# Kernel tuning notes

Measured on AMD Instinct MI355X. Metric: run time of the kernel, lower is better.

Reference implementation:

```python
import jax, jax.numpy as jnp
import numpy as np

NIN = 1024
NOUT = 1024
NHEADS = 16
DHEAD = NOUT // NHEADS


def setup_inputs() -> dict:
    key = jax.random.key(0)
    k1, k2, k3, k4 = jax.random.split(key, 4)
    y = jax.random.normal(k1, (2, 2048, NIN), dtype=jnp.float32)
    Wqkv = jax.random.normal(k2, (NIN, 3 * NOUT), dtype=jnp.float32) * (1.0 / np.sqrt(NIN))
    Wff = jax.random.normal(k3, (NOUT, NOUT), dtype=jnp.float32) * (1.0 / np.sqrt(NOUT))
    bff = jax.random.normal(k4, (NOUT,), dtype=jnp.float32) * 0.01
    return {"y": y, "Wqkv": Wqkv, "Wff": Wff, "bff": bff}


def reference(y, Wqkv, Wff, bff):
    b, n, _ = y.shape
    qkv = y @ Wqkv  # [b, n, 3*nout]
    qkv = qkv.reshape(b, n, 3, NHEADS, DHEAD).transpose(2, 0, 3, 1, 4)
    q, k, v = qkv[0], qkv[1], qkv[2]  # each [b, h, n, d]
    att = jnp.einsum('bhqd,bhkd->bhqk', q, k)
    causal = jnp.triu(jnp.ones((n, n), dtype=bool), k=1)
    att = jnp.where(causal, -jnp.inf, att)
    att = jax.nn.softmax(att / jnp.sqrt(jnp.float32(DHEAD)), axis=-1)
    ctx = jnp.einsum('bhqk,bhkd->bhqd', att, v)
    ctx = ctx.transpose(0, 2, 1, 3).reshape(b, n, NOUT)
    return ctx @ Wff + bff
```

## Files before the change

### kernel.cpp

```cpp
#include <hip/hip_runtime.h>
#include <stdint.h>

#define NHEADS 16
#define DHEAD 64
#define SEQ 2048
#define BATCH 2
#define NINF 1024
#define NOUTF 1024
#define N3 3072
#define MTOT 4096

typedef unsigned short US;
typedef __attribute__((ext_vector_type(8))) short short8;
typedef __attribute__((ext_vector_type(4))) short short4v;
typedef __attribute__((ext_vector_type(4))) float f32x4;

__device__ inline US f2bf(float f) {
  union { float f; unsigned u; } v; v.f = f;
  unsigned r = v.u + 0x7fffu + ((v.u >> 16) & 1u);
  return (US)(r >> 16);
}

__device__ inline f32x4 mfma16(short8 a, short8 b, f32x4 c) {
  return __builtin_amdgcn_mfma_f32_16x16x32_bf16(a, b, c, 0, 0, 0);
}

__device__ inline f32x4 mfma16k16(short4v a, short4v b, f32x4 c) {
  return __builtin_amdgcn_mfma_f32_16x16x16bf16_1k(a, b, c, 0, 0, 0);
}

__device__ inline void async16(const US* g, US* l) {
  __builtin_amdgcn_global_load_lds(
      (const __attribute__((address_space(1))) unsigned int*)g,
      (__attribute__((address_space(3))) unsigned int*)l, 16, 0, 0);
}

__global__ void k_convert(const float* __restrict__ src, US* __restrict__ dst, int n4) {
  int i = blockIdx.x * blockDim.x + threadIdx.x;
  if (i >= n4) return;
  float4 v = ((const float4*)src)[i];
  ushort4 o;
  o.x = f2bf(v.x); o.y = f2bf(v.y); o.z = f2bf(v.z); o.w = f2bf(v.w);
  ((ushort4*)dst)[i] = o;
}

__global__ void k_wtrans(const float* __restrict__ Wqkv, const float* __restrict__ Wff,
                         US* __restrict__ dq, US* __restrict__ df) {
  __shared__ float tile[32][33];
  int bxi = blockIdx.x;
  const float* src; US* dst; int C;
  if (bxi < 96) { src = Wqkv; dst = dq; C = N3; }
  else          { src = Wff;  dst = df; C = NOUTF; bxi -= 96; }
  int bx = bxi * 32, by = blockIdx.y * 32;
  int tx = threadIdx.x, ty = threadIdx.y;
  for (int i = 0; i < 32; i += 8)
    tile[ty + i][tx] = src[(size_t)(by + ty + i) * C + bx + tx];
  __syncthreads();
  for (int i = 0; i < 32; i += 8)
    dst[(size_t)(bx + ty + i) * 1024 + by + tx] = f2bf(tile[tx][ty + i]);
}

__global__ void k_vtrans(const US* __restrict__ src, US* __restrict__ dst) {
  __shared__ US tile[32][33];
  int bh = blockIdx.z;
  int bx = blockIdx.x * 32;
  int by = blockIdx.y * 32;
  int tx = threadIdx.x, ty = threadIdx.y;
  const US* s0 = src + (size_t)bh * SEQ * DHEAD;
  US* d0 = dst + (size_t)bh * DHEAD * SEQ;
  for (int i = 0; i < 32; i += 8)
    tile[ty + i][tx] = s0[(size_t)(by + ty + i) * DHEAD + bx + tx];
  __syncthreads();
  for (int i = 0; i < 32; i += 8)
    d0[(size_t)(bx + ty + i) * SEQ + by + tx] = tile[tx][ty + i];
}

__global__ __launch_bounds__(256) void k_gemm_qkv(
    const US* __restrict__ A,
    const US* __restrict__ Bt,
    US* __restrict__ qbuf, US* __restrict__ kbuf, US* __restrict__ vbuf) {
  __shared__ US As[128 * 32];
  __shared__ US Bs[128 * 32];
  int tid = threadIdx.x;
  int wave = tid >> 6, lane = tid & 63, lm = lane & 15, lk = lane >> 4;
  int wm = wave >> 1, wn = wave & 1;
  int mbase = blockIdx.y * 128, nbase = blockIdx.x * 128;

  f32x4 acc[4][4];
#pragma unroll
  for (int i = 0; i < 4; ++i)
#pragma unroll
    for (int j = 0; j < 4; ++j) acc[i][j] = (f32x4){0.f, 0.f, 0.f, 0.f};

  const US* ga = A + (size_t)(mbase + (tid >> 2)) * NINF + (tid & 3) * 8;
  const US* gb = Bt + (size_t)(nbase + (tid >> 2)) * NINF + (tid & 3) * 8;
  US* la = As + tid * 8;
  US* lb = Bs + tid * 8;

  for (int kt = 0; kt < NINF / 32; ++kt) {
    int ko = kt * 32;
    async16(ga + ko, la);
    async16(ga + ko + (size_t)64 * NINF, la + 64 * 32);
    async16(gb + ko, lb);
    async16(gb + ko + (size_t)64 * NINF, lb + 64 * 32);
    __syncthreads();
    short8 a[4], b[4];
#pragma unroll
    for (int i = 0; i < 4; ++i)
      a[i] = *(const short8*)(As + (wm * 64 + i * 16 + lm) * 32 + lk * 8);
#pragma unroll
    for (int j = 0; j < 4; ++j)
      b[j] = *(const short8*)(Bs + (wn * 64 + j * 16 + lm) * 32 + lk * 8);
#pragma unroll
    for (int i = 0; i < 4; ++i)
#pragma unroll
      for (int j = 0; j < 4; ++j) acc[i][j] = mfma16(a[i], b[j], acc[i][j]);
    __syncthreads();
  }

  int which = nbase >> 10;
  US* dsts = (which == 0) ? qbuf : (which == 1) ? kbuf : vbuf;
  float sc = (which == 0) ? 0.18033688011112042f : 1.f;
#pragma unroll
  for (int j = 0; j < 4; ++j) {
    int col = nbase + wn * 64 + j * 16 + lm;
    int hh = (col & 1023) >> 6;
    int d = col & 63;
#pragma unroll
    for (int i = 0; i < 4; ++i) {
#pragma unroll
      for (int r = 0; r < 4; ++r) {
        int row = mbase + wm * 64 + i * 16 + lk * 4 + r;
        int bb = row >> 11;
        int s = row & (SEQ - 1);
        int bh = bb * NHEADS + hh;
        dsts[((size_t)bh * SEQ + s) * DHEAD + d] = f2bf(acc[i][j][r] * sc);
      }
    }
  }
}

__global__ __launch_bounds__(256) void k_attn(
    const US* __restrict__ qbuf, const US* __restrict__ kbuf,
    const US* __restrict__ vtbuf, US* __restrict__ ctx) {
  __shared__ US Ks[64 * 64];
  __shared__ US Vs[64 * 64];
  int tid = threadIdx.x;
  int w = tid >> 6, lane = tid & 63;
  int lm = lane & 15, lk = lane >> 4;
  int bl = blockIdx.x;
  int xcd = bl & 7, g = bl >> 3;
  int bh = (g & 3) * 8 + xcd;
  int s = 31 - (g >> 2);
  int qb = s * 64 + w * 16;
  int nt = s + 1;

  const US* kbase = kbuf + (size_t)bh * SEQ * DHEAD;
  const US* vtb = vtbuf + (size_t)bh * DHEAD * SEQ;
  const US* qr = qbuf + ((size_t)bh * SEQ + qb + lm) * DHEAD + lk * 8;
  short8 qf0 = *(const short8*)(qr);
  short8 qf1 = *(const short8*)(qr + 32);

  int swz = ((lane & 7) ^ (lane >> 3)) * 8;
  const US* gsrc[4];
  US* ldst[4];
  int step[4];
#pragma unroll
  for (int j = 0; j < 4; ++j) {
    int u = w + 4 * j;
    if (u < 8) {
      gsrc[j] = kbase + (size_t)(u * 8 + (lane >> 3)) * DHEAD + swz;
      ldst[j] = Ks + u * 512 + lane * 8;
      step[j] = 64 * DHEAD;
    } else {
      int i = u - 8;
      gsrc[j] = vtb + (size_t)(i * 8 + (lane >> 3)) * SEQ + swz;
      ldst[j] = Vs + i * 512 + lane * 8;
      step[j] = 64;
    }
  }

  int xorv = lm & 7;
  int ck0 = ((lk) ^ xorv) * 16;
  int ck1 = ((4 + lk) ^ xorv) * 16;
  int cv[4];
#pragma unroll
  for (int kg = 0; kg < 4; ++kg)
    cv[kg] = (((kg * 2 + (lk >> 1)) ^ xorv) * 16) + (lk & 1) * 8;

  f32x4 o[4];
#pragma unroll
  for (int dg = 0; dg < 4; ++dg) o[dg] = (f32x4){0.f, 0.f, 0.f, 0.f};
  f32x4 lacc = (f32x4){0.f, 0.f, 0.f, 0.f};
  const short4v kones = {(short)0x3F80, (short)0x3F80, (short)0x3F80, (short)0x3F80};

  const char* Kc = (const char*)Ks;
  const char* Vc = (const char*)Vs;

  auto body = [&](int kg, bool dm) {
    const char* kr = Kc + (kg * 16 + lm) * 128;
    short8 ka0 = *(const short8*)(kr + ck0);
    short8 ka1 = *(const short8*)(kr + ck1);
    f32x4 st = (f32x4){0.f, 0.f, 0.f, 0.f};
    st = mfma16(ka0, qf0, st);
    st = mfma16(ka1, qf1, st);
    uint32_t ue[4];
#pragma unroll
    for (int r = 0; r < 4; ++r) {
      float v = st[r];
      if (dm && (lk * 4 + r > lm)) v = -INFINITY;
      union { float f; uint32_t u; } cv2;
      cv2.f = exp2f(v);
      ue[r] = cv2.u + 0x8000u;
    }
    union { short4v s4; uint32_t u[2]; } pk;
    pk.u[0] = __builtin_amdgcn_perm(ue[1], ue[0], 0x07060302u);
    pk.u[1] = __builtin_amdgcn_perm(ue[3], ue[2], 0x07060302u);
    lacc = mfma16k16(kones, pk.s4, lacc);
    const char* vr = Vc + lm * 128 + cv[kg];
#pragma unroll
    for (int dg = 0; dg < 4; ++dg) {
      short4v va = *(const short4v*)(vr + dg * 2048);
      o[dg] = mfma16k16(va, pk.s4, o[dg]);
    }
  };

  for (int t = 0; t < nt - 1; ++t) {
    __syncthreads();
#pragma unroll
    for (int j = 0; j < 4; ++j) async16(gsrc[j], ldst[j]);
#pragma unroll
    for (int j = 0; j < 4; ++j) gsrc[j] += step[j];
    __syncthreads();
#pragma unroll
    for (int kg = 0; kg < 4; ++kg) body(kg, false);
  }
  __syncthreads();
#pragma unroll
  for (int j = 0; j < 4; ++j) async16(gsrc[j], ldst[j]);
  __syncthreads();
  for (int kg = 0; kg < w; ++kg) body(kg, false);
  body(w, true);

  float inv = 1.f / lacc[0];

  US* crow = ctx + ((size_t)(bh >> 4) * SEQ + qb + lm) * NOUTF + (bh & 15) * DHEAD;
#pragma unroll
  for (int dg = 0; dg < 4; ++dg) {
    union { short4v s4; uint32_t u[2]; } pk;
    pk.u[0] = (uint32_t)f2bf(o[dg][0] * inv) | ((uint32_t)f2bf(o[dg][1] * inv) << 16);
    pk.u[1] = (uint32_t)f2bf(o[dg][2] * inv) | ((uint32_t)f2bf(o[dg][3] * inv) << 16);
    *(short4v*)(crow + dg * 16 + lk * 4) = pk.s4;
  }
}

__global__ __launch_bounds__(256) void k_gemm_out(
    const US* __restrict__ A, const US* __restrict__ Bt,
    const float* __restrict__ bias, float* __restrict__ out) {
  __shared__ US As[128 * 32];
  __shared__ US Bs[64 * 32];
  int tid = threadIdx.x;
  int wave = tid >> 6, lane = tid & 63, lm = lane & 15, lk = lane >> 4;
  int mbase = blockIdx.y * 128, nbase = blockIdx.x * 64;

  f32x4 acc[2][4];
#pragma unroll
  for (int i = 0; i < 2; ++i)
#pragma unroll
    for (int j = 0; j < 4; ++j) acc[i][j] = (f32x4){0.f, 0.f, 0.f, 0.f};

  const US* ga = A + (size_t)(mbase + (tid >> 2)) * NOUTF + (tid & 3) * 8;
  const US* gb = Bt + (size_t)(nbase + (tid >> 2)) * NOUTF + (tid & 3) * 8;
  US* la = As + tid * 8;
  US* lb = Bs + tid * 8;

  for (int kt = 0; kt < NOUTF / 32; ++kt) {
    int ko = kt * 32;
    async16(ga + ko, la);
    async16(ga + ko + (size_t)64 * NOUTF, la + 64 * 32);
    async16(gb + ko, lb);
    __syncthreads();
    short8 a[2], b[4];
#pragma unroll
    for (int i = 0; i < 2; ++i)
      a[i] = *(const short8*)(As + (wave * 32 + i * 16 + lm) * 32 + lk * 8);
#pragma unroll
    for (int j = 0; j < 4; ++j)
      b[j] = *(const short8*)(Bs + (j * 16 + lm) * 32 + lk * 8);
#pragma unroll
    for (int i = 0; i < 2; ++i)
#pragma unroll
      for (int j = 0; j < 4; ++j) acc[i][j] = mfma16(a[i], b[j], acc[i][j]);
    __syncthreads();
  }

#pragma unroll
  for (int j = 0; j < 4; ++j) {
    int col = nbase + j * 16 + lm;
    float bv = bias[col];
#pragma unroll
    for (int i = 0; i < 2; ++i)
#pragma unroll
      for (int r = 0; r < 4; ++r) {
        int row = mbase + wave * 32 + i * 16 + lk * 4 + r;
        out[(size_t)row * NOUTF + col] = acc[i][j][r] + bv;
      }
  }
}

extern "C" void kernel_launch(void* const* d_in, const int* in_sizes, int n_in,
                              void* d_out, int out_size, void* d_ws, size_t ws_size,
                              hipStream_t stream) {
  const float* y    = (const float*)d_in[0];
  const float* Wqkv = (const float*)d_in[1];
  const float* Wff  = (const float*)d_in[2];
  const float* bff  = (const float*)d_in[3];
  float* out = (float*)d_out;

  char* ws = (char*)d_ws;
  US* ybf   = (US*)(ws);
  US* ctx   = (US*)(ws);
  US* wqkvt = (US*)(ws + (8u << 20));
  US* wfft  = (US*)(ws + (14u << 20));
  US* qbuf  = (US*)(ws + (16u << 20));
  US* kbuf  = (US*)(ws + (24u << 20));
  US* vbuf  = (US*)(ws + (32u << 20));
  US* vtbuf = (US*)(ws + (40u << 20));

  k_convert<<<MTOT * NINF / 4 / 256, 256, 0, stream>>>(y, ybf, MTOT * NINF / 4);
  k_wtrans<<<dim3(128, 32), dim3(32, 8), 0, stream>>>(Wqkv, Wff, wqkvt, wfft);
  k_gemm_qkv<<<dim3(N3 / 128, MTOT / 128), 256, 0, stream>>>(ybf, wqkvt, qbuf, kbuf, vbuf);
  k_vtrans<<<dim3(DHEAD / 32, SEQ / 32, BATCH * NHEADS), dim3(32, 8), 0, stream>>>(vbuf, vtbuf);
  k_attn<<<dim3(1024), 256, 0, stream>>>(qbuf, kbuf, vtbuf, ctx);
  k_gemm_out<<<dim3(NOUTF / 64, MTOT / 128), 256, 0, stream>>>(ctx, wfft, bff, out);
}
```

Before: 191.7 us.

## Double-buffer K/V tiles and pair causal query tiles per attention block

```diff
diff --git a/kernel.cpp b/kernel.cpp
--- a/kernel.cpp
+++ b/kernel.cpp
@@ -143,114 +143,127 @@
 __global__ __launch_bounds__(256) void k_attn(
     const US* __restrict__ qbuf, const US* __restrict__ kbuf,
     const US* __restrict__ vtbuf, US* __restrict__ ctx) {
-  __shared__ US Ks[64 * 64];
-  __shared__ US Vs[64 * 64];
+  __shared__ US Ks[2][64 * 64];
+  __shared__ US Vs[2][64 * 64];
   int tid = threadIdx.x;
   int w = tid >> 6, lane = tid & 63;
   int lm = lane & 15, lk = lane >> 4;
   int bl = blockIdx.x;
   int xcd = bl & 7, g = bl >> 3;
   int bh = (g & 3) * 8 + xcd;
-  int s = 31 - (g >> 2);
-  int qb = s * 64 + w * 16;
-  int nt = s + 1;
+  int p = g >> 2;
 
   const US* kbase = kbuf + (size_t)bh * SEQ * DHEAD;
   const US* vtb = vtbuf + (size_t)bh * DHEAD * SEQ;
-  const US* qr = qbuf + ((size_t)bh * SEQ + qb + lm) * DHEAD + lk * 8;
-  short8 qf0 = *(const short8*)(qr);
-  short8 qf1 = *(const short8*)(qr + 32);
+  const US* q_base = qbuf + (size_t)bh * SEQ * DHEAD;
+  US* cbase = ctx + (size_t)(bh >> 4) * SEQ * NOUTF + (bh & 15) * DHEAD;
 
   int swz = ((lane & 7) ^ (lane >> 3)) * 8;
-  const US* gsrc[4];
-  US* ldst[4];
-  int step[4];
-#pragma unroll
-  for (int j = 0; j < 4; ++j) {
-    int u = w + 4 * j;
-    if (u < 8) {
-      gsrc[j] = kbase + (size_t)(u * 8 + (lane >> 3)) * DHEAD + swz;
-      ldst[j] = Ks + u * 512 + lane * 8;
-      step[j] = 64 * DHEAD;
-    } else {
-      int i = u - 8;
-      gsrc[j] = vtb + (size_t)(i * 8 + (lane >> 3)) * SEQ + swz;
-      ldst[j] = Vs + i * 512 + lane * 8;
-      step[j] = 64;
+  int u = w;
+  const US* gK0[2]; const US* gV0[2];
+  US* dK[2][2]; US* dV[2][2];
+#pragma unroll
+  for (int j = 0; j < 2; ++j) {
+    int uk = w + 4 * j;
+    int uv = w + 4 * j;
+    gK0[j] = kbase + (size_t)(uk * 8 + (lane >> 3)) * DHEAD + swz;
+    gV0[j] = vtb + (size_t)(uv * 8 + (lane >> 3)) * SEQ + swz;
+#pragma unroll
+    for (int b = 0; b < 2; ++b) {
+      dK[b][j] = Ks[b] + uk * 512 + lane * 8;
+      dV[b][j] = Vs[b] + uv * 512 + lane * 8;
     }
   }
+  (void)u;
 
   int xorv = lm & 7;
   int ck0 = ((lk) ^ xorv) * 16;
   int ck1 = ((4 + lk) ^ xorv) * 16;
-  int cv[4];
-#pragma unroll
-  for (int kg = 0; kg < 4; ++kg)
-    cv[kg] = (((kg * 2 + (lk >> 1)) ^ xorv) * 16) + (lk & 1) * 8;
-
-  f32x4 o[4];
-#pragma unroll
-  for (int dg = 0; dg < 4; ++dg) o[dg] = (f32x4){0.f, 0.f, 0.f, 0.f};
-  f32x4 lacc = (f32x4){0.f, 0.f, 0.f, 0.f};
   const short4v kones = {(short)0x3F80, (short)0x3F80, (short)0x3F80, (short)0x3F80};
 
-  const char* Kc = (const char*)Ks;
-  const char* Vc = (const char*)Vs;
-
-  auto body = [&](int kg, bool dm) {
-    const char* kr = Kc + (kg * 16 + lm) * 128;
-    short8 ka0 = *(const short8*)(kr + ck0);
-    short8 ka1 = *(const short8*)(kr + ck1);
-    f32x4 st = (f32x4){0.f, 0.f, 0.f, 0.f};
-    st = mfma16(ka0, qf0, st);
-    st = mfma16(ka1, qf1, st);
-    uint32_t ue[4];
-#pragma unroll
-    for (int r = 0; r < 4; ++r) {
-      float v = st[r];
-      if (dm && (lk * 4 + r > lm)) v = -INFINITY;
-      union { float f; uint32_t u; } cv2;
-      cv2.f = exp2f(v);
-      ue[r] = cv2.u + 0x8000u;
+  for (int half = 0; half < 2; ++half) {
+    int s = half ? p : (31 - p);
+    int qb = s * 64 + w * 16;
+    int nt = s + 1;
+
+    const US* qr = q_base + (size_t)(qb + lm) * DHEAD + lk * 8;
+    short8 qf0 = *(const short8*)(qr);
+    short8 qf1 = *(const short8*)(qr + 32);
+
+    f32x4 o[4];
+#pragma unroll
+    for (int dg = 0; dg < 4; ++dg) o[dg] = (f32x4){0.f, 0.f, 0.f, 0.f};
+    f32x4 lacc = (f32x4){0.f, 0.f, 0.f, 0.f};
+
+    const US* gK[2]; const US* gV[2];
+#pragma unroll
+    for (int j = 0; j < 2; ++j) { gK[j] = gK0[j]; gV[j] = gV0[j]; }
+
+#pragma unroll
+    for (int j = 0; j < 2; ++j) { async16(gK[j], dK[0][j]); async16(gV[j], dV[0][j]); }
+#pragma unroll
+    for (int j = 0; j < 2; ++j) { gK[j] += 64 * DHEAD; gV[j] += 64; }
+    __syncthreads();
+
+    for (int t = 0; t < nt; ++t) {
+      int cur = t & 1, nxt = cur ^ 1;
+      if (t + 1 < nt) {
+#pragma unroll
+        for (int j = 0; j < 2; ++j) { async16(gK[j], dK[nxt][j]); async16(gV[j], dV[nxt][j]); }
+#pragma unroll
+        for (int j = 0; j < 2; ++j) { gK[j] += 64 * DHEAD; gV[j] += 64; }
+      }
+
+      const char* Kc = (const char*)Ks[cur];
+      const char* Vc = (const char*)Vs[cur];
+      auto body = [&](int kg, bool dm) {
+        const char* kr = Kc + (kg * 16 + lm) * 128;
+        short8 ka0 = *(const short8*)(kr + ck0);
+        short8 ka1 = *(const short8*)(kr + ck1);
+        f32x4 st = (f32x4){0.f, 0.f, 0.f, 0.f};
+        st = mfma16(ka0, qf0, st);
+        st = mfma16(ka1, qf1, st);
+        uint32_t ue[4];
+#pragma unroll
+        for (int r = 0; r < 4; ++r) {
+          float v = st[r];
+          if (dm && (lk * 4 + r > lm)) v = -INFINITY;
+          union { float f; uint32_t u; } cv2;
+          cv2.f = exp2f(v);
+          ue[r] = cv2.u + 0x8000u;
+        }
+        union { short4v s4; uint32_t u[2]; } pk;
+        pk.u[0] = __builtin_amdgcn_perm(ue[1], ue[0], 0x07060302u);
+        pk.u[1] = __builtin_amdgcn_perm(ue[3], ue[2], 0x07060302u);
+        lacc = mfma16k16(kones, pk.s4, lacc);
+        int cvo = (((kg * 2 + (lk >> 1)) ^ xorv) * 16) + (lk & 1) * 8;
+        const char* vr = Vc + lm * 128 + cvo;
+#pragma unroll
+        for (int dg = 0; dg < 4; ++dg) {
+          short4v va = *(const short4v*)(vr + dg * 2048);
+          o[dg] = mfma16k16(va, pk.s4, o[dg]);
+        }
+      };
+
+      if (t == nt - 1) {
+        for (int kg = 0; kg < w; ++kg) body(kg, false);
+        body(w, true);
+      } else {
+#pragma unroll
+        for (int kg = 0; kg < 4; ++kg) body(kg, false);
+      }
+      __syncthreads();
     }
-    union { short4v s4; uint32_t u[2]; } pk;
-    pk.u[0] = __builtin_amdgcn_perm(ue[1], ue[0], 0x07060302u);
-    pk.u[1] = __builtin_amdgcn_perm(ue[3], ue[2], 0x07060302u);
-    lacc = mfma16k16(kones, pk.s4, lacc);
-    const char* vr = Vc + lm * 128 + cv[kg];
+
+    float inv = 1.f / lacc[0];
+    US* crow = cbase + (size_t)(qb + lm) * NOUTF;
 #pragma unroll
     for (int dg = 0; dg < 4; ++dg) {
-      short4v va = *(const short4v*)(vr + dg * 2048);
-      o[dg] = mfma16k16(va, pk.s4, o[dg]);
+      union { short4v s4; uint32_t u[2]; } pk;
+      pk.u[0] = (uint32_t)f2bf(o[dg][0] * inv) | ((uint32_t)f2bf(o[dg][1] * inv) << 16);
+      pk.u[1] = (uint32_t)f2bf(o[dg][2] * inv) | ((uint32_t)f2bf(o[dg][3] * inv) << 16);
+      *(short4v*)(crow + dg * 16 + lk * 4) = pk.s4;
     }
-  };
-
-  for (int t = 0; t < nt - 1; ++t) {
-    __syncthreads();
-#pragma unroll
-    for (int j = 0; j < 4; ++j) async16(gsrc[j], ldst[j]);
-#pragma unroll
-    for (int j = 0; j < 4; ++j) gsrc[j] += step[j];
-    __syncthreads();
-#pragma unroll
-    for (int kg = 0; kg < 4; ++kg) body(kg, false);
-  }
-  __syncthreads();
-#pragma unroll
-  for (int j = 0; j < 4; ++j) async16(gsrc[j], ldst[j]);
-  __syncthreads();
-  for (int kg = 0; kg < w; ++kg) body(kg, false);
-  body(w, true);
-
-  float inv = 1.f / lacc[0];
-
-  US* crow = ctx + ((size_t)(bh >> 4) * SEQ + qb + lm) * NOUTF + (bh & 15) * DHEAD;
-#pragma unroll
-  for (int dg = 0; dg < 4; ++dg) {
-    union { short4v s4; uint32_t u[2]; } pk;
-    pk.u[0] = (uint32_t)f2bf(o[dg][0] * inv) | ((uint32_t)f2bf(o[dg][1] * inv) << 16);
-    pk.u[1] = (uint32_t)f2bf(o[dg][2] * inv) | ((uint32_t)f2bf(o[dg][3] * inv) << 16);
-    *(short4v*)(crow + dg * 16 + lk * 4) = pk.s4;
   }
 }
 
@@ -331,6 +344,6 @@
   k_wtrans<<<dim3(128, 32), dim3(32, 8), 0, stream>>>(Wqkv, Wff, wqkvt, wfft);
   k_gemm_qkv<<<dim3(N3 / 128, MTOT / 128), 256, 0, stream>>>(ybf, wqkvt, qbuf, kbuf, vbuf);
   k_vtrans<<<dim3(DHEAD / 32, SEQ / 32, BATCH * NHEADS), dim3(32, 8), 0, stream>>>(vbuf, vtbuf);
-  k_attn<<<dim3(1024), 256, 0, stream>>>(qbuf, kbuf, vtbuf, ctx);
+  k_attn<<<dim3(512), 256, 0, stream>>>(qbuf, kbuf, vtbuf, ctx);
   k_gemm_out<<<dim3(NOUTF / 64, MTOT / 128), 256, 0, stream>>>(ctx, wfft, bff, out);
 }
```

New measurement: 194.8 us. No clear change (+1.6%).

## Have each attention wave process two 16-row query groups to reuse K/V fragments

Applied to the files above, without the earlier changes.

```diff
diff --git a/kernel.cpp b/kernel.cpp
--- a/kernel.cpp
+++ b/kernel.cpp
@@ -14,6 +14,12 @@
 typedef __attribute__((ext_vector_type(8))) short short8;
 typedef __attribute__((ext_vector_type(4))) short short4v;
 typedef __attribute__((ext_vector_type(4))) float f32x4;
+
+#if __has_builtin(__builtin_amdgcn_exp2f)
+#define EXP2(x) __builtin_amdgcn_exp2f(x)
+#else
+#define EXP2(x) exp2f(x)
+#endif
 
 __device__ inline US f2bf(float f) {
   union { float f; unsigned u; } v; v.f = f;
@@ -140,7 +146,7 @@
   }
 }
 
-__global__ __launch_bounds__(256) void k_attn(
+__global__ __launch_bounds__(128, 2) void k_attn(
     const US* __restrict__ qbuf, const US* __restrict__ kbuf,
     const US* __restrict__ vtbuf, US* __restrict__ ctx) {
   __shared__ US Ks[64 * 64];
@@ -149,108 +155,121 @@
   int w = tid >> 6, lane = tid & 63;
   int lm = lane & 15, lk = lane >> 4;
   int bl = blockIdx.x;
-  int xcd = bl & 7, g = bl >> 3;
-  int bh = (g & 3) * 8 + xcd;
-  int s = 31 - (g >> 2);
-  int qb = s * 64 + w * 16;
+  int xcd = bl & 7, g2 = bl >> 3;
+  int bh = (g2 & 3) * 8 + xcd;
+  int s = 31 - (g2 >> 2);
+  int qb = s * 64 + w * 32;
   int nt = s + 1;
 
   const US* kbase = kbuf + (size_t)bh * SEQ * DHEAD;
   const US* vtb = vtbuf + (size_t)bh * DHEAD * SEQ;
-  const US* qr = qbuf + ((size_t)bh * SEQ + qb + lm) * DHEAD + lk * 8;
-  short8 qf0 = *(const short8*)(qr);
-  short8 qf1 = *(const short8*)(qr + 32);
+  const US* q_base = qbuf + (size_t)bh * SEQ * DHEAD;
+
+  short8 qf[2][2];
+#pragma unroll
+  for (int g = 0; g < 2; ++g) {
+    const US* qr = q_base + (size_t)(qb + g * 16 + lm) * DHEAD + lk * 8;
+    qf[g][0] = *(const short8*)(qr);
+    qf[g][1] = *(const short8*)(qr + 32);
+  }
 
   int swz = ((lane & 7) ^ (lane >> 3)) * 8;
-  const US* gsrc[4];
-  US* ldst[4];
-  int step[4];
+  const US* gK[4]; const US* gV[4];
+  US* dKl[4]; US* dVl[4];
 #pragma unroll
   for (int j = 0; j < 4; ++j) {
-    int u = w + 4 * j;
-    if (u < 8) {
-      gsrc[j] = kbase + (size_t)(u * 8 + (lane >> 3)) * DHEAD + swz;
-      ldst[j] = Ks + u * 512 + lane * 8;
-      step[j] = 64 * DHEAD;
-    } else {
-      int i = u - 8;
-      gsrc[j] = vtb + (size_t)(i * 8 + (lane >> 3)) * SEQ + swz;
-      ldst[j] = Vs + i * 512 + lane * 8;
-      step[j] = 64;
-    }
+    int u = w * 4 + j;
+    gK[j] = kbase + (size_t)(u * 8 + (lane >> 3)) * DHEAD + swz;
+    dKl[j] = Ks + u * 512 + lane * 8;
+    gV[j] = vtb + (size_t)(u * 8 + (lane >> 3)) * SEQ + swz;
+    dVl[j] = Vs + u * 512 + lane * 8;
   }
 
   int xorv = lm & 7;
   int ck0 = ((lk) ^ xorv) * 16;
   int ck1 = ((4 + lk) ^ xorv) * 16;
-  int cv[4];
-#pragma unroll
-  for (int kg = 0; kg < 4; ++kg)
-    cv[kg] = (((kg * 2 + (lk >> 1)) ^ xorv) * 16) + (lk & 1) * 8;
-
-  f32x4 o[4];
-#pragma unroll
-  for (int dg = 0; dg < 4; ++dg) o[dg] = (f32x4){0.f, 0.f, 0.f, 0.f};
-  f32x4 lacc = (f32x4){0.f, 0.f, 0.f, 0.f};
   const short4v kones = {(short)0x3F80, (short)0x3F80, (short)0x3F80, (short)0x3F80};
+
+  f32x4 o[2][4];
+#pragma unroll
+  for (int g = 0; g < 2; ++g)
+#pragma unroll
+    for (int dg = 0; dg < 4; ++dg) o[g][dg] = (f32x4){0.f, 0.f, 0.f, 0.f};
+  f32x4 lacc[2];
+  lacc[0] = (f32x4){0.f, 0.f, 0.f, 0.f};
+  lacc[1] = (f32x4){0.f, 0.f, 0.f, 0.f};
 
   const char* Kc = (const char*)Ks;
   const char* Vc = (const char*)Vs;
 
-  auto body = [&](int kg, bool dm) {
+  auto body = [&](int kg, bool act0, bool dm0, bool dm1) {
     const char* kr = Kc + (kg * 16 + lm) * 128;
     short8 ka0 = *(const short8*)(kr + ck0);
     short8 ka1 = *(const short8*)(kr + ck1);
-    f32x4 st = (f32x4){0.f, 0.f, 0.f, 0.f};
-    st = mfma16(ka0, qf0, st);
-    st = mfma16(ka1, qf1, st);
-    uint32_t ue[4];
-#pragma unroll
-    for (int r = 0; r < 4; ++r) {
-      float v = st[r];
-      if (dm && (lk * 4 + r > lm)) v = -INFINITY;
-      union { float f; uint32_t u; } cv2;
-      cv2.f = exp2f(v);
-      ue[r] = cv2.u + 0x8000u;
-    }
-    union { short4v s4; uint32_t u[2]; } pk;
-    pk.u[0] = __builtin_amdgcn_perm(ue[1], ue[0], 0x07060302u);
-    pk.u[1] = __builtin_amdgcn_perm(ue[3], ue[2], 0x07060302u);
-    lacc = mfma16k16(kones, pk.s4, lacc);
-    const char* vr = Vc + lm * 128 + cv[kg];
+    short4v pk[2];
+    bool act[2] = {act0, true};
+    bool dm[2] = {dm0, dm1};
+#pragma unroll
+    for (int g = 0; g < 2; ++g) {
+      if (!act[g]) continue;
+      f32x4 st = (f32x4){0.f, 0.f, 0.f, 0.f};
+      st = mfma16(ka0, qf[g][0], st);
+      st = mfma16(ka1, qf[g][1], st);
+      uint32_t ue[4];
+#pragma unroll
+      for (int r = 0; r < 4; ++r) {
+        float v = st[r];
+        if (dm[g] && (lk * 4 + r > lm)) v = -INFINITY;
+        union { float f; uint32_t u; } cv2;
+        cv2.f = EXP2(v);
+        ue[r] = cv2.u + 0x8000u;
+      }
+      union { short4v s4; uint32_t u[2]; } pz;
+      pz.u[0] = __builtin_amdgcn_perm(ue[1], ue[0], 0x07060302u);
+      pz.u[1] = __builtin_amdgcn_perm(ue[3], ue[2], 0x07060302u);
+      pk[g] = pz.s4;
+      lacc[g] = mfma16k16(kones, pk[g], lacc[g]);
+    }
+    int cvo = (((kg * 2 + (lk >> 1)) ^ xorv) * 16) + (lk & 1) * 8;
+    const char* vr = Vc + lm * 128 + cvo;
 #pragma unroll
     for (int dg = 0; dg < 4; ++dg) {
       short4v va = *(const short4v*)(vr + dg * 2048);
-      o[dg] = mfma16k16(va, pk.s4, o[dg]);
+      if (act0) o[0][dg] = mfma16k16(va, pk[0], o[0][dg]);
+      o[1][dg] = mfma16k16(va, pk[1], o[1][dg]);
     }
   };
 
-  for (int t = 0; t < nt - 1; ++t) {
-    __syncthreads();
-#pragma unroll
-    for (int j = 0; j < 4; ++j) async16(gsrc[j], ldst[j]);
-#pragma unroll
-    for (int j = 0; j < 4; ++j) gsrc[j] += step[j];
-    __syncthreads();
-#pragma unroll
-    for (int kg = 0; kg < 4; ++kg) body(kg, false);
-  }
-  __syncthreads();
-#pragma unroll
-  for (int j = 0; j < 4; ++j) async16(gsrc[j], ldst[j]);
-  __syncthreads();
-  for (int kg = 0; kg < w; ++kg) body(kg, false);
-  body(w, true);
-
-  float inv = 1.f / lacc[0];
-
-  US* crow = ctx + ((size_t)(bh >> 4) * SEQ + qb + lm) * NOUTF + (bh & 15) * DHEAD;
-#pragma unroll
-  for (int dg = 0; dg < 4; ++dg) {
-    union { short4v s4; uint32_t u[2]; } pk;
-    pk.u[0] = (uint32_t)f2bf(o[dg][0] * inv) | ((uint32_t)f2bf(o[dg][1] * inv) << 16);
-    pk.u[1] = (uint32_t)f2bf(o[dg][2] * inv) | ((uint32_t)f2bf(o[dg][3] * inv) << 16);
-    *(short4v*)(crow + dg * 16 + lk * 4) = pk.s4;
+  for (int t = 0; t < nt; ++t) {
+    __syncthreads();
+#pragma unroll
+    for (int j = 0; j < 4; ++j) { async16(gK[j], dKl[j]); async16(gV[j], dVl[j]); }
+#pragma unroll
+    for (int j = 0; j < 4; ++j) { gK[j] += 64 * DHEAD; gV[j] += 64; }
+    __syncthreads();
+
+    if (t < nt - 1) {
+#pragma unroll
+      for (int kg = 0; kg < 4; ++kg) body(kg, true, false, false);
+    } else {
+      int kmax = 2 * w + 1;
+      for (int kg = 0; kg <= kmax; ++kg)
+        body(kg, kg <= 2 * w, kg == 2 * w, kg == kmax);
+    }
+  }
+
+  US* cb = ctx + (size_t)(bh >> 4) * SEQ * NOUTF + (bh & 15) * DHEAD;
+#pragma unroll
+  for (int g = 0; g < 2; ++g) {
+    float inv = 1.f / lacc[g][0];
+    US* crow = cb + (size_t)(qb + g * 16 + lm) * NOUTF;
+#pragma unroll
+    for (int dg = 0; dg < 4; ++dg) {
+      union { short4v s4; uint32_t u[2]; } pz;
+      pz.u[0] = (uint32_t)f2bf(o[g][dg][0] * inv) | ((uint32_t)f2bf(o[g][dg][1] * inv) << 16);
+      pz.u[1] = (uint32_t)f2bf(o[g][dg][2] * inv) | ((uint32_t)f2bf(o[g][dg][3] * inv) << 16);
+      *(short4v*)(crow + dg * 16 + lk * 4) = pz.s4;
+    }
   }
 }
 
@@ -331,6 +350,6 @@
   k_wtrans<<<dim3(128, 32), dim3(32, 8), 0, stream>>>(Wqkv, Wff, wqkvt, wfft);
   k_gemm_qkv<<<dim3(N3 / 128, MTOT / 128), 256, 0, stream>>>(ybf, wqkvt, qbuf, kbuf, vbuf);
   k_vtrans<<<dim3(DHEAD / 32, SEQ / 32, BATCH * NHEADS), dim3(32, 8), 0, stream>>>(vbuf, vtbuf);
-  k_attn<<<dim3(1024), 256, 0, stream>>>(qbuf, kbuf, vtbuf, ctx);
+  k_attn<<<dim3(1024), 128, 0, stream>>>(qbuf, kbuf, vtbuf, ctx);
   k_gemm_out<<<dim3(NOUTF / 64, MTOT / 128), 256, 0, stream>>>(ctx, wfft, bff, out);
 }
```

Result: no change. 194.1 us (+1.3%).
